# Kernel tuning notes

Measured on AMD Instinct MI355X. Metric: run time of the kernel, lower is better.

The kernel has to match this reference:

```python
import jax, jax.numpy as jnp
import numpy as np

B, N, C = 16, 1024, 256
NH, DH = 8, 32          # dense attention heads
NHD, P = 8, 4           # deformable heads / sampling points
Hs = Ws = 32            # value spatial grid (N == Hs*Ws)
HID = 1024              # mlp hidden = 4*C


def setup_inputs() -> dict:
    key = jax.random.key(0)
    ks = jax.random.split(key, 16)
    rn = lambda i, shape, s=1.0: jax.random.normal(ks[i], shape, jnp.float32) * s
    return {
        "x": rn(0, (B, N, C)),
        "ref": jax.random.uniform(ks[1], (B, N, 2), jnp.float32),
        "value": rn(2, (B, N, C)),
        "ln1_w": jnp.ones((C,), jnp.float32), "ln1_b": jnp.zeros((C,), jnp.float32),
        "ln2_w": jnp.ones((C,), jnp.float32), "ln2_b": jnp.zeros((C,), jnp.float32),
        "ln3_w": jnp.ones((C,), jnp.float32), "ln3_b": jnp.zeros((C,), jnp.float32),
        "qkv_w": rn(3, (3 * C, C), 0.05),
        "proj_w": rn(4, (C, C), 0.05), "proj_b": jnp.zeros((C,), jnp.float32),
        "off_w": rn(5, (NHD * P * 2, C), 0.01), "off_b": rn(6, (NHD * P * 2,), 0.5),
        "aw_w": rn(7, (NHD * P, C), 0.01), "aw_b": jnp.zeros((NHD * P,), jnp.float32),
        "vproj_w": rn(8, (C, C), 0.05), "vproj_b": jnp.zeros((C,), jnp.float32),
        "oproj_w": rn(9, (C, C), 0.05), "oproj_b": jnp.zeros((C,), jnp.float32),
        "fc1_w": rn(10, (HID, C), 0.05), "fc1_b": jnp.zeros((HID,), jnp.float32),
        "fc2_w": rn(11, (C, HID), 0.05), "fc2_b": jnp.zeros((C,), jnp.float32),
    }


def _ln(x, w, b):
    m = x.mean(-1, keepdims=True)
    v = ((x - m) ** 2).mean(-1, keepdims=True)
    return (x - m) * jax.lax.rsqrt(v + 1e-5) * w + b


def _attn(x, qkv_w, proj_w, proj_b):
    qkv = (x @ qkv_w.T).reshape(B, N, 3, NH, DH)
    q, k, v = qkv[:, :, 0], qkv[:, :, 1], qkv[:, :, 2]
    a = jnp.einsum('bqhd,bkhd->bhqk', q, k) * (DH ** -0.5)
    a = jax.nn.softmax(a, axis=-1)
    o = jnp.einsum('bhqk,bkhd->bqhd', a, v).reshape(B, N, C)
    return o @ proj_w.T + proj_b


def _deform(q, ref, value, off_w, off_b, aw_w, aw_b, vproj_w, vproj_b, oproj_w, oproj_b):
    # single-level MS deformable attention (Deformable-DETR style)
    v = (value @ vproj_w.T + vproj_b).reshape(B, Hs * Ws, NHD, DH)
    off = (q @ off_w.T + off_b).reshape(B, N, NHD, P, 2)
    aw = jax.nn.softmax((q @ aw_w.T + aw_b).reshape(B, N, NHD, P), axis=-1)
    norm = jnp.array([Ws, Hs], jnp.float32)
    loc = ref[:, :, None, None, :] + off / norm  # [B,N,NHD,P,2] normalized coords
    gx = loc[..., 0] * Ws - 0.5
    gy = loc[..., 1] * Hs - 0.5
    x0 = jnp.floor(gx); y0 = jnp.floor(gy)
    lx = gx - x0; ly = gy - y0
    x0i = x0.astype(jnp.int32); y0i = y0.astype(jnp.int32)
    b_idx = jnp.arange(B)[:, None, None, None]
    h_idx = jnp.arange(NHD)[None, None, :, None]

    def gather(xi, yi):
        valid = ((xi >= 0) & (xi < Ws) & (yi >= 0) & (yi < Hs)).astype(jnp.float32)
        idx = jnp.clip(yi, 0, Hs - 1) * Ws + jnp.clip(xi, 0, Ws - 1)
        return v[b_idx, idx, h_idx] * valid[..., None]  # [B,N,NHD,P,DH]

    s = (gather(x0i, y0i) * ((1 - lx) * (1 - ly))[..., None]
         + gather(x0i + 1, y0i) * (lx * (1 - ly))[..., None]
         + gather(x0i, y0i + 1) * ((1 - lx) * ly)[..., None]
         + gather(x0i + 1, y0i + 1) * (lx * ly)[..., None])
    out = (s * aw[..., None]).sum(axis=3).reshape(B, N, C)
    return out @ oproj_w.T + oproj_b


def reference(x, ref, value, ln1_w, ln1_b, ln2_w, ln2_b, ln3_w, ln3_b,
              qkv_w, proj_w, proj_b, off_w, off_b, aw_w, aw_b,
              vproj_w, vproj_b, oproj_w, oproj_b, fc1_w, fc1_b, fc2_w, fc2_b):
    x = x + _attn(_ln(x, ln1_w, ln1_b), qkv_w, proj_w, proj_b)
    x = x + _deform(_ln(x, ln2_w, ln2_b), ref, value,
                    off_w, off_b, aw_w, aw_b, vproj_w, vproj_b, oproj_w, oproj_b)
    h = jax.nn.gelu(_ln(x, ln3_w, ln3_b) @ fc1_w.T + fc1_b, approximate=False) @ fc2_w.T + fc2_b
    return x + h
```

## Files before the change

kernel.cpp:

```cpp
#include <hip/hip_runtime.h>
#include <hip/hip_bf16.h>

#define Bq   16
#define Nq   1024
#define Cq   256
#define NHq  8
#define DHq  32
#define HIDq 1024
#define BNq  (Bq * Nq)

typedef float f32x4 __attribute__((ext_vector_type(4)));
typedef short bf16x8 __attribute__((ext_vector_type(8)));
typedef unsigned short ushort_t;

__device__ __forceinline__ unsigned int f2bf(float f) {
    unsigned int u = __builtin_bit_cast(unsigned int, f);
    u = (u + 0x7fffu + ((u >> 16) & 1u)) >> 16;
    return u & 0xffffu;
}
__device__ __forceinline__ unsigned int packbf2(float a, float b) {
    unsigned int ua = __builtin_bit_cast(unsigned int, a) + 0x8000u;
    unsigned int ub = __builtin_bit_cast(unsigned int, b) + 0x8000u;
    return __builtin_amdgcn_perm(ub, ua, 0x07060302);
}
__device__ __forceinline__ unsigned int cvtpk_bf16(float lo, float hi) {
    unsigned int r;
    asm("v_cvt_pk_bf16_f32 %0, %1, %2" : "=v"(r) : "v"(lo), "v"(hi));
    return r;
}
__device__ __forceinline__ float gelu_t(float x) {
    float y = x * (0.7978845608028654f + 0.035677408136300125f * x * x);
    float e = __builtin_amdgcn_exp2f(y * 2.8853900817779268f);
    return x - x / (1.f + e);
}

typedef __attribute__((address_space(1))) const unsigned int* gas_u32;
typedef __attribute__((address_space(3))) unsigned int* las_u32;
__device__ __forceinline__ void gload16(const void* g, void* l) {
    __builtin_amdgcn_global_load_lds((gas_u32)g, (las_u32)l, 16, 0, 0);
}

struct CastSeg { const float* src; ushort_t* dst; int nblk; int n; };
struct CastArgs { CastSeg s[9]; };

__global__ __launch_bounds__(256) void castm(CastArgs a) {
    int bid = blockIdx.x;
    int seg = 0, acc = 0;
    for (seg = 0; seg < 9; seg++) {
        if (bid < acc + a.s[seg].nblk) break;
        acc += a.s[seg].nblk;
    }
    const CastSeg sg = a.s[seg];
    int i = (bid - acc) * 1024 + threadIdx.x * 4;
    if (i < sg.n) {
        float4 v = *(const float4*)(sg.src + i);
        uint2 u;
        u.x = packbf2(v.x, v.y);
        u.y = packbf2(v.z, v.w);
        *(uint2*)(sg.dst + i) = u;
    }
}

__global__ __launch_bounds__(256) void ln_kernel(const float* __restrict__ X,
                                                 const float* __restrict__ w,
                                                 const float* __restrict__ b,
                                                 ushort_t* __restrict__ Y) {
    int wave = threadIdx.x >> 6, lane = threadIdx.x & 63;
    int t = blockIdx.x * 4 + wave;
    float4 v = *(const float4*)(X + (size_t)t * Cq + lane * 4);
    float s = v.x + v.y + v.z + v.w;
#pragma unroll
    for (int d = 1; d < 64; d <<= 1) s += __shfl_xor(s, d);
    float mean = s * (1.f / 256.f);
    float4 dv = {v.x - mean, v.y - mean, v.z - mean, v.w - mean};
    float q = dv.x * dv.x + dv.y * dv.y + dv.z * dv.z + dv.w * dv.w;
#pragma unroll
    for (int d = 1; d < 64; d <<= 1) q += __shfl_xor(q, d);
    float rs = rsqrtf(q * (1.f / 256.f) + 1e-5f);
    float4 wv = *(const float4*)(w + lane * 4);
    float4 bv = *(const float4*)(b + lane * 4);
    uint2 u;
    u.x = packbf2(dv.x * rs * wv.x + bv.x, dv.y * rs * wv.y + bv.y);
    u.y = packbf2(dv.z * rs * wv.z + bv.z, dv.w * rs * wv.w + bv.w);
    *(uint2*)(Y + (size_t)t * Cq + lane * 4) = u;
}

template <int OMODE, bool GELU_, bool RESID, int KT>
__global__ __launch_bounds__(256) void mgemm(const ushort_t* __restrict__ A,
                                             const ushort_t* __restrict__ W,
                                             const float* __restrict__ bias,
                                             const float* __restrict__ R,
                                             void* __restrict__ OutP,
                                             int M, int Nn) {
    __shared__ __align__(16) ushort_t Al[8192];
    __shared__ __align__(16) ushort_t Bl[8192];
    int m0 = blockIdx.x * 128, n0 = blockIdx.y * 128;
    int tid = threadIdx.x;
    int w = tid >> 6, lane = tid & 63;
    int l15 = lane & 15, quad = lane >> 4;
    int wrow = w >> 1, wcol = w & 1;

    f32x4 acc[4][4];
#pragma unroll
    for (int i = 0; i < 4; i++)
#pragma unroll
        for (int j = 0; j < 4; j++) acc[i][j] = (f32x4){0.f, 0.f, 0.f, 0.f};

    const ushort_t* gA0 = A + (size_t)(m0 + lane) * KT + w * 8;
    const ushort_t* gA1 = A + (size_t)(m0 + 64 + lane) * KT + w * 8;
    const ushort_t* gB0 = W + (size_t)(n0 + lane) * KT + w * 8;
    const ushort_t* gB1 = W + (size_t)(n0 + 64 + lane) * KT + w * 8;
    ushort_t* lA0 = &Al[(w * 128) * 8];
    ushort_t* lA1 = &Al[(w * 128 + 64) * 8];
    ushort_t* lB0 = &Bl[(w * 128) * 8];
    ushort_t* lB1 = &Bl[(w * 128 + 64) * 8];
    constexpr int BUFO = 4096;

    gload16(gA0, lA0);
    gload16(gA1, lA1);
    gload16(gB0, lB0);
    gload16(gB1, lB1);
    __syncthreads();

    constexpr int NT = KT / 32;
#pragma unroll
    for (int t = 0; t < NT; t++) {
        const int cur = (t & 1) * BUFO;
        const int nxt = ((t + 1) & 1) * BUFO;
        if (t + 1 < NT) {
            gload16(gA0 + (t + 1) * 32, lA0 + nxt);
            gload16(gA1 + (t + 1) * 32, lA1 + nxt);
            gload16(gB0 + (t + 1) * 32, lB0 + nxt);
            gload16(gB1 + (t + 1) * 32, lB1 + nxt);
        }
        bf16x8 aF[4], bF[4];
#pragma unroll
        for (int i = 0; i < 4; i++)
            aF[i] = *(const bf16x8*)&Al[cur + (quad * 128 + wrow * 64 + i * 16 + l15) * 8];
#pragma unroll
        for (int j = 0; j < 4; j++)
            bF[j] = *(const bf16x8*)&Bl[cur + (quad * 128 + wcol * 64 + j * 16 + l15) * 8];
#pragma unroll
        for (int i = 0; i < 4; i++)
#pragma unroll
            for (int j = 0; j < 4; j++)
                acc[i][j] = __builtin_amdgcn_mfma_f32_16x16x32_bf16(bF[j], aF[i], acc[i][j], 0, 0, 0);
        __syncthreads();
    }

#pragma unroll
    for (int i = 0; i < 4; i++) {
        int mg = m0 + wrow * 64 + i * 16 + l15;
#pragma unroll
        for (int j = 0; j < 4; j++) {
            int ng = n0 + wcol * 64 + j * 16 + quad * 4;
            f32x4 rv = acc[i][j];
            if constexpr (OMODE == 1) {
                int which = ng >> 8;
                int h = (ng >> 5) & 7;
                int d = ng & 31;
                int bb = mg >> 10, nn = mg & 1023;
                ushort_t* qb = (ushort_t*)OutP;
                if (which == 2) {
                    size_t dst = 2 * (size_t)BNq * Cq +
                                 ((size_t)(bb * 8 + h) * 32 + d) * 1024 + nn;
#pragma unroll
                    for (int r = 0; r < 4; r++)
                        qb[dst + (size_t)r * 1024] = (ushort_t)f2bf(rv[r]);
                } else {
                    if (which == 0) {
                        const float sc = 0.17677669529663687f * 1.4426950408889634f;
                        rv[0] *= sc; rv[1] *= sc; rv[2] *= sc; rv[3] *= sc;
                    }
                    size_t dst = (size_t)which * ((size_t)BNq * Cq) +
                                 ((size_t)(bb * 8 + h) * 1024 + nn) * 32 + d;
                    uint2 pk;
                    pk.x = packbf2(rv[0], rv[1]);
                    pk.y = packbf2(rv[2], rv[3]);
                    *(uint2*)(qb + dst) = pk;
                }
            } else if constexpr (OMODE == 3) {
                if (ng >= 96) continue;
                if (ng < 64) {
                    float4 bv = *(const float4*)(bias + ng);
                    rv[0] += bv.x; rv[1] += bv.y; rv[2] += bv.z; rv[3] += bv.w;
                    *(float4*)((float*)OutP + (size_t)mg * 64 + ng) =
                        make_float4(rv[0], rv[1], rv[2], rv[3]);
                } else {
                    float4 bv = *(const float4*)(R + (ng - 64));
                    rv[0] += bv.x; rv[1] += bv.y; rv[2] += bv.z; rv[3] += bv.w;
                    *(float4*)((float*)OutP + (size_t)BNq * 64 + (size_t)mg * 32 + (ng - 64)) =
                        make_float4(rv[0], rv[1], rv[2], rv[3]);
                }
            } else {
                if (bias) {
                    float4 bv = *(const float4*)(bias + ng);
                    rv[0] += bv.x; rv[1] += bv.y; rv[2] += bv.z; rv[3] += bv.w;
                }
                if (GELU_) {
#pragma unroll
                    for (int r = 0; r < 4; r++) rv[r] = gelu_t(rv[r]);
                }
                if constexpr (OMODE == 2) {
                    uint2 pk;
                    pk.x = packbf2(rv[0], rv[1]);
                    pk.y = packbf2(rv[2], rv[3]);
                    *(uint2*)((ushort_t*)OutP + (size_t)mg * Nn + ng) = pk;
                } else {
                    if (RESID) {
                        float4 rr = *(const float4*)(R + (size_t)mg * Nn + ng);
                        rv[0] += rr.x; rv[1] += rr.y; rv[2] += rr.z; rv[3] += rr.w;
                    }
                    *(float4*)((float*)OutP + (size_t)mg * Nn + ng) =
                        make_float4(rv[0], rv[1], rv[2], rv[3]);
                }
            }
        }
    }
}

__global__ __launch_bounds__(256, 4) void attn_mfma(const ushort_t* __restrict__ Qb,
                                                    const ushort_t* __restrict__ Kb,
                                                    const ushort_t* __restrict__ Vtg,
                                                    ushort_t* __restrict__ o) {
    int bh = blockIdx.x;
    int b = bh >> 3, h = bh & 7;
    int q0 = blockIdx.y * 128;
    int tid = threadIdx.x;
    int wave = tid >> 6, lane = tid & 63;
    int l15 = lane & 15, quad = lane >> 4;

    __shared__ __align__(16) ushort_t Ks[2][64][40];
    __shared__ __align__(16) ushort_t Vs[2][32][88];
    __shared__ __align__(16) ushort_t Ps[4][32][72];

    const size_t hb = (size_t)bh * 32768;

    bf16x8 qfrag[2];
#pragma unroll
    for (int g = 0; g < 2; g++)
        qfrag[g] = *(const bf16x8*)(Qb + hb + (size_t)(q0 + wave * 32 + g * 16 + l15) * 32 + quad * 8);

    f32x4 oa[2][2];
#pragma unroll
    for (int g = 0; g < 2; g++)
#pragma unroll
        for (int t = 0; t < 2; t++) oa[g][t] = (f32x4){0.f, 0.f, 0.f, 0.f};
    f32x4 ls[2];
    ls[0] = (f32x4){0.f, 0.f, 0.f, 0.f};
    ls[1] = (f32x4){0.f, 0.f, 0.f, 0.f};

    bf16x8 ones;
#pragma unroll
    for (int i = 0; i < 8; i++) ones[i] = (short)0x3F80;

    int krow = tid >> 2, kch = tid & 3;
    int vrow = tid >> 3, vch = tid & 7;
    const ushort_t* kgp = Kb + hb + (size_t)krow * 32 + kch * 8;
    const ushort_t* vgp = Vtg + hb + (size_t)vrow * 1024 + vch * 8;

    bf16x8 kreg = *(const bf16x8*)kgp;
    bf16x8 vreg = *(const bf16x8*)vgp;

#pragma unroll 2
    for (int kt = 0; kt < 16; kt++) {
        const int cur = kt & 1;
        *(bf16x8*)&Ks[cur][krow][kch * 8] = kreg;
        *(bf16x8*)&Vs[cur][vrow][vch * 8] = vreg;
        __syncthreads();
        if (kt < 15) {
            kreg = *(const bf16x8*)(kgp + (kt + 1) * 2048);
            vreg = *(const bf16x8*)(vgp + (kt + 1) * 64);
        }

        bf16x8 kf[4];
#pragma unroll
        for (int kg = 0; kg < 4; kg++)
            kf[kg] = *(const bf16x8*)&Ks[cur][kg * 16 + l15][quad * 8];

        const f32x4 z = {0.f, 0.f, 0.f, 0.f};
#pragma unroll
        for (int g = 0; g < 2; g++) {
#pragma unroll
            for (int kg = 0; kg < 4; kg++) {
                f32x4 st = __builtin_amdgcn_mfma_f32_16x16x32_bf16(kf[kg], qfrag[g], z, 0, 0, 0);
                float e0 = __builtin_amdgcn_exp2f(st[0]);
                float e1 = __builtin_amdgcn_exp2f(st[1]);
                float e2 = __builtin_amdgcn_exp2f(st[2]);
                float e3 = __builtin_amdgcn_exp2f(st[3]);
                uint2 pk;
                pk.x = cvtpk_bf16(e0, e1);
                pk.y = cvtpk_bf16(e2, e3);
                *(uint2*)&Ps[wave][g * 16 + l15][kg * 16 + quad * 4] = pk;
            }
        }

        __builtin_amdgcn_s_setprio(1);
#pragma unroll
        for (int c = 0; c < 2; c++) {
            bf16x8 vb0 = *(const bf16x8*)&Vs[cur][l15][c * 32 + quad * 8];
            bf16x8 vb1 = *(const bf16x8*)&Vs[cur][16 + l15][c * 32 + quad * 8];
#pragma unroll
            for (int g = 0; g < 2; g++) {
                bf16x8 pa = *(const bf16x8*)&Ps[wave][g * 16 + l15][c * 32 + quad * 8];
                oa[g][0] = __builtin_amdgcn_mfma_f32_16x16x32_bf16(pa, vb0, oa[g][0], 0, 0, 0);
                oa[g][1] = __builtin_amdgcn_mfma_f32_16x16x32_bf16(pa, vb1, oa[g][1], 0, 0, 0);
                ls[g]    = __builtin_amdgcn_mfma_f32_16x16x32_bf16(pa, ones, ls[g], 0, 0, 0);
            }
        }
        __builtin_amdgcn_s_setprio(0);
    }

#pragma unroll
    for (int g = 0; g < 2; g++) {
#pragma unroll
        for (int r = 0; r < 4; r++) {
            float inv = 1.f / ls[g][r];
            int q = q0 + wave * 32 + g * 16 + quad * 4 + r;
            ushort_t* orow = o + ((size_t)(b * 1024 + q)) * 256 + h * 32;
            orow[l15] = (ushort_t)f2bf(oa[g][0][r] * inv);
            orow[l15 + 16] = (ushort_t)f2bf(oa[g][1][r] * inv);
        }
    }
}

__global__ __launch_bounds__(256) void deform_kernel(const float* __restrict__ ref,
                                                     const float* __restrict__ off,
                                                     const float* __restrict__ awl,
                                                     const float* __restrict__ v,
                                                     ushort_t* __restrict__ out) {
    int t = blockIdx.x;
    int b = t >> 10;
    int tid = threadIdx.x;
    int h = tid >> 5, d = tid & 31;

    float rx = ref[(size_t)t * 2 + 0];
    float ry = ref[(size_t)t * 2 + 1];
    const float* offr = off + (size_t)t * 64 + h * 8;
    const float* awr = awl + (size_t)t * 32 + h * 4;

    float L0 = awr[0], L1 = awr[1], L2 = awr[2], L3 = awr[3];
    float mm = fmaxf(fmaxf(L0, L1), fmaxf(L2, L3));
    float e0 = __expf(L0 - mm), e1 = __expf(L1 - mm), e2 = __expf(L2 - mm), e3 = __expf(L3 - mm);
    float inv = 1.f / (e0 + e1 + e2 + e3);
    float aw[4] = {e0 * inv, e1 * inv, e2 * inv, e3 * inv};

    const float* vb = v + (size_t)b * Nq * Cq + h * 32 + d;

    float s = 0.f;
#pragma unroll
    for (int p = 0; p < 4; p++) {
        float gx = rx * 32.f + offr[p * 2 + 0] - 0.5f;
        float gy = ry * 32.f + offr[p * 2 + 1] - 0.5f;
        float x0f = floorf(gx), y0f = floorf(gy);
        float lx = gx - x0f, ly = gy - y0f;
        int x0 = (int)x0f, y0 = (int)y0f;
        auto g = [&](int xi, int yi) -> float {
            if (xi < 0 || xi > 31 || yi < 0 || yi > 31) return 0.f;
            return vb[(size_t)(yi * 32 + xi) * Cq];
        };
        float sp = g(x0, y0) * (1.f - lx) * (1.f - ly)
                 + g(x0 + 1, y0) * lx * (1.f - ly)
                 + g(x0, y0 + 1) * (1.f - lx) * ly
                 + g(x0 + 1, y0 + 1) * lx * ly;
        s += aw[p] * sp;
    }
    out[(size_t)t * Cq + h * 32 + d] = (ushort_t)f2bf(s);
}

extern "C" void kernel_launch(void* const* d_in, const int* in_sizes, int n_in,
                              void* d_out, int out_size, void* d_ws, size_t ws_size,
                              hipStream_t stream) {
    const size_t S = (size_t)BNq * Cq;
    float* ws = (float*)d_ws;
    float* X = ws;
    ushort_t* Ybf = (ushort_t*)(ws + S);
    ushort_t* Wbf = (ushort_t*)(ws + S + S / 2);

    ushort_t* Wqkv   = Wbf;
    ushort_t* Wproj  = Wbf + 196608;
    ushort_t* Woff   = Wbf + 262144;
    ushort_t* Waw    = Wbf + 278528;
    ushort_t* Wvproj = Wbf + 286720;
    ushort_t* Woproj = Wbf + 352256;
    ushort_t* Wfc1   = Wbf + 417792;
    ushort_t* Wfc2   = Wbf + 679936;

    ushort_t* QKVbf = (ushort_t*)(ws + 2 * S);
    ushort_t* O1bf  = (ushort_t*)(ws + 2 * S + 3 * S / 2);
    float* Vb   = ws + 2 * S + S / 2;
    float* OffB = ws + 2 * S + 3 * S / 2;
    float* AwB  = OffB + (size_t)BNq * 64;
    ushort_t* Sbbf = (ushort_t*)(AwB + (size_t)BNq * 32);
    ushort_t* Hbbf = (ushort_t*)(ws + 2 * S);
    ushort_t* Valbf = (ushort_t*)(ws + 9 * S / 2);

    auto fp = [&](int i) { return (const float*)d_in[i]; };
    const float* x_in = fp(0);

    CastArgs ca;
    ca.s[0] = {fp(9),  Wqkv,   192, 196608};
    ca.s[1] = {fp(10), Wproj,  64,  65536};
    ca.s[2] = {fp(12), Woff,   16,  16384};
    ca.s[3] = {fp(14), Waw,    8,   8192};
    ca.s[4] = {fp(16), Wvproj, 64,  65536};
    ca.s[5] = {fp(18), Woproj, 64,  65536};
    ca.s[6] = {fp(20), Wfc1,   256, 262144};
    ca.s[7] = {fp(22), Wfc2,   256, 262144};
    ca.s[8] = {fp(2),  Valbf,  4096, (int)S};
    castm<<<5016, 256, 0, stream>>>(ca);

    ln_kernel<<<BNq / 4, 256, 0, stream>>>(x_in, fp(3), fp(4), Ybf);
    mgemm<1, false, false, 256><<<dim3(128, 6), 256, 0, stream>>>(
        Ybf, Wqkv, nullptr, nullptr, QKVbf, BNq, 768);
    attn_mfma<<<dim3(128, 8), 256, 0, stream>>>(
        QKVbf, QKVbf + S, QKVbf + 2 * S, O1bf);
    mgemm<0, false, true, 256><<<dim3(128, 2), 256, 0, stream>>>(
        O1bf, Wproj, fp(11), x_in, X, BNq, 256);

    ln_kernel<<<BNq / 4, 256, 0, stream>>>(X, fp(5), fp(6), Ybf);
    mgemm<0, false, false, 256><<<dim3(128, 2), 256, 0, stream>>>(
        Valbf, Wvproj, fp(17), nullptr, Vb, BNq, 256);
    mgemm<3, false, false, 256><<<dim3(128, 1), 256, 0, stream>>>(
        Ybf, Woff, fp(13), fp(15), OffB, BNq, 96);
    deform_kernel<<<BNq, 256, 0, stream>>>(fp(1), OffB, AwB, Vb, Sbbf);
    mgemm<0, false, true, 256><<<dim3(128, 2), 256, 0, stream>>>(
        Sbbf, Woproj, fp(19), X, X, BNq, 256);

    ln_kernel<<<BNq / 4, 256, 0, stream>>>(X, fp(7), fp(8), Ybf);
    mgemm<2, true, false, 256><<<dim3(128, 8), 256, 0, stream>>>(
        Ybf, Wfc1, fp(21), nullptr, Hbbf, BNq, 1024);
    mgemm<0, false, true, 1024><<<dim3(128, 2), 256, 0, stream>>>(
        Hbbf, Wfc2, fp(23), X, d_out, BNq, 256);
}
```

Measured before the change: 337.7 us.

## Add BN=64 GEMM tile variant and switch to single-buffered 64-wide K steps

The GEMM kernel gets a BN template parameter. All launches now use 128x64 tiles, which doubles the grid size so more blocks can spread across the CUs. The K loop also changes from a double-buffered 32-wide prefetch pipeline to a single-buffered 64-wide step with two MFMA sub-steps per barrier. That halves the number of barriers but drops the overlap of global loads with compute, and the smaller N tile lowers data reuse per block.

```diff
diff --git a/kernel.cpp b/kernel.cpp
--- a/kernel.cpp
+++ b/kernel.cpp
@@ -85,72 +85,78 @@
     *(uint2*)(Y + (size_t)t * Cq + lane * 4) = u;
 }
 
-template <int OMODE, bool GELU_, bool RESID, int KT>
+template <int OMODE, bool GELU_, bool RESID, int KT, int BN>
 __global__ __launch_bounds__(256) void mgemm(const ushort_t* __restrict__ A,
                                              const ushort_t* __restrict__ W,
                                              const float* __restrict__ bias,
                                              const float* __restrict__ R,
                                              void* __restrict__ OutP,
                                              int M, int Nn) {
+    constexpr int MI = (BN == 128) ? 4 : 2;
+    constexpr int WM = (BN == 128) ? 64 : 32;
     __shared__ __align__(16) ushort_t Al[8192];
-    __shared__ __align__(16) ushort_t Bl[8192];
-    int m0 = blockIdx.x * 128, n0 = blockIdx.y * 128;
+    __shared__ __align__(16) ushort_t Bl[BN * 64];
+    int m0 = blockIdx.x * 128, n0 = blockIdx.y * BN;
     int tid = threadIdx.x;
     int w = tid >> 6, lane = tid & 63;
     int l15 = lane & 15, quad = lane >> 4;
-    int wrow = w >> 1, wcol = w & 1;
-
-    f32x4 acc[4][4];
-#pragma unroll
-    for (int i = 0; i < 4; i++)
+    int wrow = (BN == 128) ? (w >> 1) : w;
+    int wcol = (BN == 128) ? (w & 1) : 0;
+
+    f32x4 acc[MI][4];
+#pragma unroll
+    for (int i = 0; i < MI; i++)
 #pragma unroll
         for (int j = 0; j < 4; j++) acc[i][j] = (f32x4){0.f, 0.f, 0.f, 0.f};
 
     const ushort_t* gA0 = A + (size_t)(m0 + lane) * KT + w * 8;
-    const ushort_t* gA1 = A + (size_t)(m0 + 64 + lane) * KT + w * 8;
+    const ushort_t* gA1 = gA0 + (size_t)64 * KT;
     const ushort_t* gB0 = W + (size_t)(n0 + lane) * KT + w * 8;
-    const ushort_t* gB1 = W + (size_t)(n0 + 64 + lane) * KT + w * 8;
-    ushort_t* lA0 = &Al[(w * 128) * 8];
-    ushort_t* lA1 = &Al[(w * 128 + 64) * 8];
-    ushort_t* lB0 = &Bl[(w * 128) * 8];
-    ushort_t* lB1 = &Bl[(w * 128 + 64) * 8];
-    constexpr int BUFO = 4096;
-
-    gload16(gA0, lA0);
-    gload16(gA1, lA1);
-    gload16(gB0, lB0);
-    gload16(gB1, lB1);
-    __syncthreads();
-
-    constexpr int NT = KT / 32;
-#pragma unroll
-    for (int t = 0; t < NT; t++) {
-        const int cur = (t & 1) * BUFO;
-        const int nxt = ((t + 1) & 1) * BUFO;
-        if (t + 1 < NT) {
-            gload16(gA0 + (t + 1) * 32, lA0 + nxt);
-            gload16(gA1 + (t + 1) * 32, lA1 + nxt);
-            gload16(gB0 + (t + 1) * 32, lB0 + nxt);
-            gload16(gB1 + (t + 1) * 32, lB1 + nxt);
-        }
-        bf16x8 aF[4], bF[4];
-#pragma unroll
-        for (int i = 0; i < 4; i++)
-            aF[i] = *(const bf16x8*)&Al[cur + (quad * 128 + wrow * 64 + i * 16 + l15) * 8];
-#pragma unroll
-        for (int j = 0; j < 4; j++)
-            bF[j] = *(const bf16x8*)&Bl[cur + (quad * 128 + wcol * 64 + j * 16 + l15) * 8];
-#pragma unroll
-        for (int i = 0; i < 4; i++)
+    const ushort_t* gB1 = gB0 + (size_t)64 * KT;
+    ushort_t* lA0  = &Al[w * 1024];
+    ushort_t* lA1  = lA0 + 512;
+    ushort_t* lA0h = &Al[(w + 4) * 1024];
+    ushort_t* lA1h = lA0h + 512;
+    ushort_t* lB0  = &Bl[w * (BN * 8)];
+    ushort_t* lB0h = &Bl[(w + 4) * (BN * 8)];
+    ushort_t* lB1  = lB0 + 512;
+    ushort_t* lB1h = lB0h + 512;
+
+#pragma unroll
+    for (int k0 = 0; k0 < KT; k0 += 64) {
+        gload16(gA0 + k0, lA0);
+        gload16(gA1 + k0, lA1);
+        gload16(gA0 + k0 + 32, lA0h);
+        gload16(gA1 + k0 + 32, lA1h);
+        gload16(gB0 + k0, lB0);
+        gload16(gB0 + k0 + 32, lB0h);
+        if constexpr (BN == 128) {
+            gload16(gB1 + k0, lB1);
+            gload16(gB1 + k0 + 32, lB1h);
+        }
+        __syncthreads();
+
+#pragma unroll
+        for (int ks = 0; ks < 2; ks++) {
+            bf16x8 aF[MI], bF[4];
+#pragma unroll
+            for (int i = 0; i < MI; i++)
+                aF[i] = *(const bf16x8*)&Al[((ks * 4 + quad) * 128 + wrow * WM + i * 16 + l15) * 8];
 #pragma unroll
             for (int j = 0; j < 4; j++)
-                acc[i][j] = __builtin_amdgcn_mfma_f32_16x16x32_bf16(bF[j], aF[i], acc[i][j], 0, 0, 0);
+                bF[j] = *(const bf16x8*)&Bl[((ks * 4 + quad) * BN + wcol * 64 + j * 16 + l15) * 8];
+#pragma unroll
+            for (int i = 0; i < MI; i++)
+#pragma unroll
+                for (int j = 0; j < 4; j++)
+                    acc[i][j] = __builtin_amdgcn_mfma_f32_16x16x32_bf16(bF[j], aF[i], acc[i][j], 0, 0, 0);
+        }
         __syncthreads();
     }
 
 #pragma unroll
-    for (int i = 0; i < 4; i++) {
-        int mg = m0 + wrow * 64 + i * 16 + l15;
+    for (int i = 0; i < MI; i++) {
+        int mg = m0 + wrow * WM + i * 16 + l15;
 #pragma unroll
         for (int j = 0; j < 4; j++) {
             int ng = n0 + wcol * 64 + j * 16 + quad * 4;
@@ -411,25 +417,25 @@
     castm<<<5016, 256, 0, stream>>>(ca);
 
     ln_kernel<<<BNq / 4, 256, 0, stream>>>(x_in, fp(3), fp(4), Ybf);
-    mgemm<1, false, false, 256><<<dim3(128, 6), 256, 0, stream>>>(
+    mgemm<1, false, false, 256, 64><<<dim3(128, 12), 256, 0, stream>>>(
         Ybf, Wqkv, nullptr, nullptr, QKVbf, BNq, 768);
     attn_mfma<<<dim3(128, 8), 256, 0, stream>>>(
         QKVbf, QKVbf + S, QKVbf + 2 * S, O1bf);
-    mgemm<0, false, true, 256><<<dim3(128, 2), 256, 0, stream>>>(
+    mgemm<0, false, true, 256, 64><<<dim3(128, 4), 256, 0, stream>>>(
         O1bf, Wproj, fp(11), x_in, X, BNq, 256);
 
     ln_kernel<<<BNq / 4, 256, 0, stream>>>(X, fp(5), fp(6), Ybf);
-    mgemm<0, false, false, 256><<<dim3(128, 2), 256, 0, stream>>>(
+    mgemm<0, false, false, 256, 64><<<dim3(128, 4), 256, 0, stream>>>(
         Valbf, Wvproj, fp(17), nullptr, Vb, BNq, 256);
-    mgemm<3, false, false, 256><<<dim3(128, 1), 256, 0, stream>>>(
+    mgemm<3, false, false, 256, 64><<<dim3(128, 2), 256, 0, stream>>>(
         Ybf, Woff, fp(13), fp(15), OffB, BNq, 96);
     deform_kernel<<<BNq, 256, 0, stream>>>(fp(1), OffB, AwB, Vb, Sbbf);
-    mgemm<0, false, true, 256><<<dim3(128, 2), 256, 0, stream>>>(
+    mgemm<0, false, true, 256, 64><<<dim3(128, 4), 256, 0, stream>>>(
         Sbbf, Woproj, fp(19), X, X, BNq, 256);
 
     ln_kernel<<<BNq / 4, 256, 0, stream>>>(X, fp(7), fp(8), Ybf);
-    mgemm<2, true, false, 256><<<dim3(128, 8), 256, 0, stream>>>(
+    mgemm<2, true, false, 256, 64><<<dim3(128, 16), 256, 0, stream>>>(
         Ybf, Wfc1, fp(21), nullptr, Hbbf, BNq, 1024);
-    mgemm<0, false, true, 1024><<<dim3(128, 2), 256, 0, stream>>>(
+    mgemm<0, false, true, 1024, 64><<<dim3(128, 4), 256, 0, stream>>>(
         Hbbf, Wfc2, fp(23), X, d_out, BNq, 256);
 }
```

Result: no change. 334.8 us (-0.9%).

## Replace LDS-staged GEMM with direct global-to-register fragment loads

Applied to the files above, without the earlier changes.

The GEMM kernel no longer stages A and W tiles through shared memory with global_load_lds and barriers. Each wave now loads its MFMA fragments straight from global memory into registers, double-buffered across K steps. The block tile changes to 256x64, with four waves each owning a 64-row strip. This removes LDS traffic and __syncthreads, but cross-wave reuse now depends on cache rather than LDS, which raises global and L2 load traffic.

```diff
diff --git a/kernel.cpp b/kernel.cpp
--- a/kernel.cpp
+++ b/kernel.cpp
@@ -32,12 +32,6 @@
     float y = x * (0.7978845608028654f + 0.035677408136300125f * x * x);
     float e = __builtin_amdgcn_exp2f(y * 2.8853900817779268f);
     return x - x / (1.f + e);
-}
-
-typedef __attribute__((address_space(1))) const unsigned int* gas_u32;
-typedef __attribute__((address_space(3))) unsigned int* las_u32;
-__device__ __forceinline__ void gload16(const void* g, void* l) {
-    __builtin_amdgcn_global_load_lds((gas_u32)g, (las_u32)l, 16, 0, 0);
 }
 
 struct CastSeg { const float* src; ushort_t* dst; int nblk; int n; };
@@ -86,19 +80,26 @@
 }
 
 template <int OMODE, bool GELU_, bool RESID, int KT>
-__global__ __launch_bounds__(256) void mgemm(const ushort_t* __restrict__ A,
+__global__ __launch_bounds__(256) void sgemm(const ushort_t* __restrict__ A,
                                              const ushort_t* __restrict__ W,
                                              const float* __restrict__ bias,
                                              const float* __restrict__ R,
                                              void* __restrict__ OutP,
                                              int M, int Nn) {
-    __shared__ __align__(16) ushort_t Al[8192];
-    __shared__ __align__(16) ushort_t Bl[8192];
-    int m0 = blockIdx.x * 128, n0 = blockIdx.y * 128;
     int tid = threadIdx.x;
     int w = tid >> 6, lane = tid & 63;
     int l15 = lane & 15, quad = lane >> 4;
-    int wrow = w >> 1, wcol = w & 1;
+    int m0 = blockIdx.x * 256 + w * 64;
+    int n0 = blockIdx.y * 64;
+
+    const ushort_t* pA[4];
+    const ushort_t* pB[4];
+#pragma unroll
+    for (int i = 0; i < 4; i++)
+        pA[i] = A + (size_t)(m0 + i * 16 + l15) * KT + quad * 8;
+#pragma unroll
+    for (int j = 0; j < 4; j++)
+        pB[j] = W + (size_t)(n0 + j * 16 + l15) * KT + quad * 8;
 
     f32x4 acc[4][4];
 #pragma unroll
@@ -106,54 +107,36 @@
 #pragma unroll
         for (int j = 0; j < 4; j++) acc[i][j] = (f32x4){0.f, 0.f, 0.f, 0.f};
 
-    const ushort_t* gA0 = A + (size_t)(m0 + lane) * KT + w * 8;
-    const ushort_t* gA1 = A + (size_t)(m0 + 64 + lane) * KT + w * 8;
-    const ushort_t* gB0 = W + (size_t)(n0 + lane) * KT + w * 8;
-    const ushort_t* gB1 = W + (size_t)(n0 + 64 + lane) * KT + w * 8;
-    ushort_t* lA0 = &Al[(w * 128) * 8];
-    ushort_t* lA1 = &Al[(w * 128 + 64) * 8];
-    ushort_t* lB0 = &Bl[(w * 128) * 8];
-    ushort_t* lB1 = &Bl[(w * 128 + 64) * 8];
-    constexpr int BUFO = 4096;
-
-    gload16(gA0, lA0);
-    gload16(gA1, lA1);
-    gload16(gB0, lB0);
-    gload16(gB1, lB1);
-    __syncthreads();
-
-    constexpr int NT = KT / 32;
-#pragma unroll
-    for (int t = 0; t < NT; t++) {
-        const int cur = (t & 1) * BUFO;
-        const int nxt = ((t + 1) & 1) * BUFO;
-        if (t + 1 < NT) {
-            gload16(gA0 + (t + 1) * 32, lA0 + nxt);
-            gload16(gA1 + (t + 1) * 32, lA1 + nxt);
-            gload16(gB0 + (t + 1) * 32, lB0 + nxt);
-            gload16(gB1 + (t + 1) * 32, lB1 + nxt);
-        }
-        bf16x8 aF[4], bF[4];
+    constexpr int NK = KT / 32;
+    bf16x8 aF[2][4], bF[2][4];
+#pragma unroll
+    for (int i = 0; i < 4; i++) {
+        aF[0][i] = *(const bf16x8*)(pA[i]);
+        bF[0][i] = *(const bf16x8*)(pB[i]);
+    }
+#pragma unroll
+    for (int ks = 0; ks < NK; ks++) {
+        const int cur = ks & 1, nxt = cur ^ 1;
+        if (ks + 1 < NK) {
+#pragma unroll
+            for (int i = 0; i < 4; i++) {
+                aF[nxt][i] = *(const bf16x8*)(pA[i] + (ks + 1) * 32);
+                bF[nxt][i] = *(const bf16x8*)(pB[i] + (ks + 1) * 32);
+            }
+        }
 #pragma unroll
         for (int i = 0; i < 4; i++)
-            aF[i] = *(const bf16x8*)&Al[cur + (quad * 128 + wrow * 64 + i * 16 + l15) * 8];
-#pragma unroll
-        for (int j = 0; j < 4; j++)
-            bF[j] = *(const bf16x8*)&Bl[cur + (quad * 128 + wcol * 64 + j * 16 + l15) * 8];
-#pragma unroll
-        for (int i = 0; i < 4; i++)
 #pragma unroll
             for (int j = 0; j < 4; j++)
-                acc[i][j] = __builtin_amdgcn_mfma_f32_16x16x32_bf16(bF[j], aF[i], acc[i][j], 0, 0, 0);
-        __syncthreads();
+                acc[i][j] = __builtin_amdgcn_mfma_f32_16x16x32_bf16(bF[cur][j], aF[cur][i], acc[i][j], 0, 0, 0);
     }
 
 #pragma unroll
     for (int i = 0; i < 4; i++) {
-        int mg = m0 + wrow * 64 + i * 16 + l15;
+        int mg = m0 + i * 16 + l15;
 #pragma unroll
         for (int j = 0; j < 4; j++) {
-            int ng = n0 + wcol * 64 + j * 16 + quad * 4;
+            int ng = n0 + j * 16 + quad * 4;
             f32x4 rv = acc[i][j];
             if constexpr (OMODE == 1) {
                 int which = ng >> 8;
@@ -411,25 +394,25 @@
     castm<<<5016, 256, 0, stream>>>(ca);
 
     ln_kernel<<<BNq / 4, 256, 0, stream>>>(x_in, fp(3), fp(4), Ybf);
-    mgemm<1, false, false, 256><<<dim3(128, 6), 256, 0, stream>>>(
+    sgemm<1, false, false, 256><<<dim3(64, 12), 256, 0, stream>>>(
         Ybf, Wqkv, nullptr, nullptr, QKVbf, BNq, 768);
     attn_mfma<<<dim3(128, 8), 256, 0, stream>>>(
         QKVbf, QKVbf + S, QKVbf + 2 * S, O1bf);
-    mgemm<0, false, true, 256><<<dim3(128, 2), 256, 0, stream>>>(
+    sgemm<0, false, true, 256><<<dim3(64, 4), 256, 0, stream>>>(
         O1bf, Wproj, fp(11), x_in, X, BNq, 256);
 
     ln_kernel<<<BNq / 4, 256, 0, stream>>>(X, fp(5), fp(6), Ybf);
-    mgemm<0, false, false, 256><<<dim3(128, 2), 256, 0, stream>>>(
+    sgemm<0, false, false, 256><<<dim3(64, 4), 256, 0, stream>>>(
         Valbf, Wvproj, fp(17), nullptr, Vb, BNq, 256);
-    mgemm<3, false, false, 256><<<dim3(128, 1), 256, 0, stream>>>(
+    sgemm<3, false, false, 256><<<dim3(64, 2), 256, 0, stream>>>(
         Ybf, Woff, fp(13), fp(15), OffB, BNq, 96);
     deform_kernel<<<BNq, 256, 0, stream>>>(fp(1), OffB, AwB, Vb, Sbbf);
-    mgemm<0, false, true, 256><<<dim3(128, 2), 256, 0, stream>>>(
+    sgemm<0, false, true, 256><<<dim3(64, 4), 256, 0, stream>>>(
         Sbbf, Woproj, fp(19), X, X, BNq, 256);
 
     ln_kernel<<<BNq / 4, 256, 0, stream>>>(X, fp(7), fp(8), Ybf);
-    mgemm<2, true, false, 256><<<dim3(128, 8), 256, 0, stream>>>(
+    sgemm<2, true, false, 256><<<dim3(64, 16), 256, 0, stream>>>(
         Ybf, Wfc1, fp(21), nullptr, Hbbf, BNq, 1024);
-    mgemm<0, false, true, 1024><<<dim3(128, 2), 256, 0, stream>>>(
+    sgemm<0, false, true, 1024><<<dim3(64, 4), 256, 0, stream>>>(
         Hbbf, Wfc2, fp(23), X, d_out, BNq, 256);
 }
```

Measured after the change: 386.8 us. 14.5% more time.
